# Kernel tuning notes

Hardware: AMD Instinct MI355X
Metric: run time of the kernel (lower is better)

## Reference

```python
import jax, jax.numpy as jnp
import numpy as np

B, S, H, NH = 2, 2048, 1024, 16
D = H // NH

def setup_inputs() -> dict:
    key = jax.random.key(0)
    ks = jax.random.split(key, 9)
    s = 1.0 / np.sqrt(H)
    return {
        "x": jax.random.normal(ks[0], (B, S, H), jnp.float32),
        "wq": jax.random.uniform(ks[1], (H, H), jnp.float32, -s, s),
        "bq": jax.random.uniform(ks[2], (H,), jnp.float32, -s, s),
        "wk": jax.random.uniform(ks[3], (H, H), jnp.float32, -s, s),
        "bk": jax.random.uniform(ks[4], (H,), jnp.float32, -s, s),
        "wv": jax.random.uniform(ks[5], (H, H), jnp.float32, -s, s),
        "bv": jax.random.uniform(ks[6], (H,), jnp.float32, -s, s),
        "wo": jax.random.uniform(ks[7], (H, H), jnp.float32, -s, s),
        "bo": jax.random.uniform(ks[8], (H,), jnp.float32, -s, s),
    }

def _split_heads(t):
    # [B, S, H] -> [B, NH, S, D]
    return t.reshape(B, S, NH, D).transpose(0, 2, 1, 3)

def reference(x, wq, bq, wk, bk, wv, bv, wo, bo):
    q = _split_heads(x @ wq.T + bq)
    k = _split_heads(x @ wk.T + bk)
    v = _split_heads(x @ wv.T + bv)
    scores = jnp.einsum('bhqd,bhkd->bhqk', q, k) / jnp.sqrt(jnp.float32(D))
    attn = jax.nn.softmax(scores, axis=-1)  # full [B,NH,S,S] materialized as in source
    ctx = jnp.einsum('bhqk,bhkd->bhqd', attn, v)
    concat = ctx.transpose(0, 2, 1, 3).reshape(B, S, H)
    return concat @ wo.T + bo
```

## Files before the change

kernel.cpp:

```cpp
#include <hip/hip_runtime.h>
#include <cstdint>

typedef unsigned short u16;
typedef __attribute__((ext_vector_type(8))) short short8;
typedef __attribute__((ext_vector_type(4))) float f32x4;
typedef __attribute__((ext_vector_type(4))) unsigned short ushort4v;
typedef __attribute__((ext_vector_type(4))) unsigned int uint4v;

#if __has_builtin(__builtin_amdgcn_exp2f)
#define EXP2F(x) __builtin_amdgcn_exp2f(x)
#else
#define EXP2F(x) exp2f(x)
#endif

__device__ inline u16 f2bf(float f) {
  union { float f; unsigned u; } v; v.f = f;
  unsigned u = v.u;
  return (u16)((u + 0x7fffu + ((u >> 16) & 1u)) >> 16);
}

__device__ inline float bf2f(u16 h) {
  union { unsigned u; float f; } v; v.u = ((unsigned)h) << 16;
  return v.f;
}

__device__ inline unsigned pk2bf_fast(float a, float b) {
  union { float f; unsigned u; } ua, ub; ua.f = a; ub.f = b;
  return __builtin_amdgcn_perm(ub.u + 0x8000u, ua.u + 0x8000u, 0x07060302u);
}

__device__ inline void gl2lds16(const void* g, void* l) {
  __builtin_amdgcn_global_load_lds(
      (const __attribute__((address_space(1))) unsigned int*)(unsigned long long)(uintptr_t)g,
      (__attribute__((address_space(3))) unsigned int*)(unsigned int)(uintptr_t)l,
      16, 0, 0);
}


__global__ __launch_bounds__(256) void cvt_kernel(
    const float* __restrict__ x,
    const float* __restrict__ wq, const float* __restrict__ wk,
    const float* __restrict__ wv,
    u16* __restrict__ xb, u16* __restrict__ wqb, u16* __restrict__ wkb,
    u16* __restrict__ wvb) {
  const int y = blockIdx.y;
  const int Q = 1 << 20;
  const float* src;
  u16* dst;
  if (y < 4)       { src = x + y * Q; dst = xb + y * Q; }
  else if (y == 4) { src = wq; dst = wqb; }
  else if (y == 5) { src = wk; dst = wkb; }
  else             { src = wv; dst = wvb; }
  const int i = (blockIdx.x * 256 + threadIdx.x) * 8;
  float4 a = *(const float4*)(src + i);
  float4 b = *(const float4*)(src + i + 4);
  short8 o;
  o[0] = (short)f2bf(a.x); o[1] = (short)f2bf(a.y);
  o[2] = (short)f2bf(a.z); o[3] = (short)f2bf(a.w);
  o[4] = (short)f2bf(b.x); o[5] = (short)f2bf(b.y);
  o[6] = (short)f2bf(b.z); o[7] = (short)f2bf(b.w);
  const int j = (i & ~63) | (((((i >> 3) & 7) ^ ((i >> 10) & 7))) << 3);
  *(short8*)(dst + j) = o;
}

__global__ __launch_bounds__(256, 2) void gemm_qkv(
    const u16* __restrict__ xb,
    const u16* __restrict__ wqb, const u16* __restrict__ wkb, const u16* __restrict__ wvb,
    const float* __restrict__ bq, const float* __restrict__ bk, const float* __restrict__ bv,
    u16* __restrict__ qo, u16* __restrict__ ko, u16* __restrict__ vto) {
  __shared__ u16 smem[40960];
  u16* As = smem;
  u16* Bs = smem + 16384;
  const int tid = threadIdx.x, lane = tid & 63;
  const int wid = tid >> 6;
  const int l15 = lane & 15, lg = lane >> 4;
  const int m0 = blockIdx.y * 128, n0 = blockIdx.x * 64;
  const int sw = ((l15 & 7) << 3);
  const u16* Wz[3] = {wqb, wkb, wvb};

  f32x4 acc[3][2][4] = {};

#pragma unroll
  for (int i = 0; i < 4; ++i) {
    int c = i * 256 + tid;
    gl2lds16(xb + (m0 + (c >> 3)) * 1024 + (c & 7) * 8, As + c * 8);
  }
#pragma unroll
  for (int z = 0; z < 3; ++z)
#pragma unroll
    for (int i = 0; i < 2; ++i) {
      int c = i * 256 + tid;
      gl2lds16(Wz[z] + (n0 + (c >> 3)) * 1024 + (c & 7) * 8, Bs + z * 4096 + c * 8);
    }

  for (int k0 = 0; k0 < 1024; k0 += 64) {
    const int p = (k0 >> 6) & 1;
    __syncthreads();
    if (k0 < 960) {
      u16* An = As + (1 - p) * 8192;
      u16* Bn = Bs + (1 - p) * 12288;
#pragma unroll
      for (int i = 0; i < 4; ++i) {
        int c = i * 256 + tid;
        gl2lds16(xb + (m0 + (c >> 3)) * 1024 + k0 + 64 + (c & 7) * 8, An + c * 8);
      }
#pragma unroll
      for (int z = 0; z < 3; ++z)
#pragma unroll
        for (int i = 0; i < 2; ++i) {
          int c = i * 256 + tid;
          gl2lds16(Wz[z] + (n0 + (c >> 3)) * 1024 + k0 + 64 + (c & 7) * 8, Bn + z * 4096 + c * 8);
        }
    }
    const u16* Ap = As + p * 8192;
    const u16* Bp = Bs + p * 12288;
#pragma unroll
    for (int kk = 0; kk < 2; ++kk) {
      short8 af[2], bf[3][4];
#pragma unroll
      for (int mb = 0; mb < 2; ++mb)
        af[mb] = *(const short8*)(Ap + (wid * 32 + mb * 16 + l15) * 64 + ((((kk * 4 + lg) << 3)) ^ sw));
#pragma unroll
      for (int z = 0; z < 3; ++z)
#pragma unroll
        for (int nb = 0; nb < 4; ++nb)
          bf[z][nb] = *(const short8*)(Bp + z * 4096 + (nb * 16 + l15) * 64 + ((((kk * 4 + lg) << 3)) ^ sw));
#pragma unroll
      for (int z = 0; z < 3; ++z)
#pragma unroll
        for (int mb = 0; mb < 2; ++mb)
#pragma unroll
          for (int nb = 0; nb < 4; ++nb)
            acc[z][mb][nb] = __builtin_amdgcn_mfma_f32_16x16x32_bf16(af[mb], bf[z][nb], acc[z][mb][nb], 0, 0, 0);
    }
  }

  const float cexp = 0.18033688011112042f;

#pragma unroll
  for (int mb = 0; mb < 2; ++mb)
#pragma unroll
    for (int nb = 0; nb < 4; ++nb)
#pragma unroll
      for (int r = 0; r < 4; ++r) {
        int m = m0 + wid * 32 + mb * 16 + lg * 4 + r;
        int n = n0 + nb * 16 + l15;
        float v = (acc[0][mb][nb][r] + bq[n]) * cexp;
        int b = m >> 11, s = m & 2047, hh = n >> 6, d = n & 63;
        qo[((b * 16 + hh) * 2048 + s) * 64 + d] = f2bf(v);
      }

#pragma unroll
  for (int mb = 0; mb < 2; ++mb)
#pragma unroll
    for (int nb = 0; nb < 4; ++nb)
#pragma unroll
      for (int r = 0; r < 4; ++r) {
        int m = m0 + wid * 32 + mb * 16 + lg * 4 + r;
        int n = n0 + nb * 16 + l15;
        float v = acc[1][mb][nb][r] + bk[n];
        int b = m >> 11, s = m & 2047, hh = n >> 6, d = n & 63;
        int dcol = (((d >> 3) ^ (s & 7)) << 3) | (d & 7);
        ko[((b * 16 + hh) * 2048 + s) * 64 + dcol] = f2bf(v);
      }

  __syncthreads();
  {
    u16* wbuf = smem + (wid >> 1) * 4608;
#pragma unroll
    for (int mb = 0; mb < 2; ++mb)
#pragma unroll
      for (int nb = 0; nb < 4; ++nb) {
        int n = n0 + nb * 16 + l15;
        float bn = bv[n];
        int dl = nb * 16 + l15;
#pragma unroll
        for (int r = 0; r < 4; ++r) {
          int sig = (wid & 1) * 32 + lg * 8 + mb * 4 + r;
          wbuf[dl * 72 + sig] = f2bf(acc[2][mb][nb][r] + bn);
        }
      }
    __syncthreads();
    int hh = n0 >> 6;
    int bb = m0 >> 11;
    int sbase = m0 & 2047;
#pragma unroll
    for (int i = 0; i < 4; ++i) {
      int idx = i * 256 + tid;
      int p2 = idx >> 9, rem = idx & 511;
      int dl = rem >> 3, c = rem & 7;
      short8 vv = *(const short8*)(smem + p2 * 4608 + dl * 72 + c * 8);
      int cs = c ^ (dl & 7);
      *(short8*)(vto + ((bb * 16 + hh) * 64 + dl) * 2048 + sbase + p2 * 64 + cs * 8) = vv;
    }
  }
}

__global__ __launch_bounds__(256, 2) void attn_kernel(
    const u16* __restrict__ qg, const u16* __restrict__ kg,
    const u16* __restrict__ vtg, u16* __restrict__ ctxg, u16* __restrict__ ctxlg) {
  const int h = blockIdx.x, qt = blockIdx.y, b = blockIdx.z;
  const int bh = b * 16 + h;
  const u16* Qg = qg + (bh * 2048 + qt * 128) * 64;
  const u16* Kg = kg + bh * 2048 * 64;
  const u16* Vg = vtg + bh * 64 * 2048;

  __shared__ unsigned SP32[128 * 72];
  __shared__ u16 KV[2][8192];

  const int tid = threadIdx.x, lane = tid & 63, wid = tid >> 6;
  const int l15 = lane & 15, lg = lane >> 4;
  const int row0 = wid * 32;
  const int sw = ((l15 & 7) << 3);

  short8 qf[2][2];
#pragma unroll
  for (int qtile = 0; qtile < 2; ++qtile)
#pragma unroll
    for (int kk = 0; kk < 2; ++kk)
      qf[qtile][kk] = *(const short8*)(Qg + (row0 + qtile * 16 + l15) * 64 + kk * 32 + lg * 8);

  short8 ones8;
#pragma unroll
  for (int j = 0; j < 8; ++j) ones8[j] = (short)0x3F80;

#pragma unroll
  for (int i = 0; i < 2; ++i) {
    int c = i * 256 + tid;
    gl2lds16(Kg + c * 8, &KV[0][c * 8]);
    gl2lds16(Vg + (c >> 3) * 2048 + (c & 7) * 8, &KV[0][4096 + c * 8]);
  }

  f32x4 acc[4][2] = {};
  f32x4 accl[2] = {};

  for (int kt = 0; kt < 32; ++kt) {
    const int p = kt & 1;
    __syncthreads();
    if (kt < 31) {
#pragma unroll
      for (int i = 0; i < 2; ++i) {
        int c = i * 256 + tid;
        gl2lds16(Kg + (kt + 1) * 4096 + c * 8, &KV[1 - p][c * 8]);
        gl2lds16(Vg + (c >> 3) * 2048 + (kt + 1) * 64 + (c & 7) * 8, &KV[1 - p][4096 + c * 8]);
      }
    }
    const u16* Ks = &KV[p][0];
    const u16* Vts = &KV[p][4096];

    f32x4 sc[4][2] = {};
#pragma unroll
    for (int kk = 0; kk < 2; ++kk) {
      short8 kf[4];
#pragma unroll
      for (int ktile = 0; ktile < 4; ++ktile)
        kf[ktile] = *(const short8*)(Ks + (ktile * 16 + l15) * 64 + ((((kk * 4 + lg) << 3)) ^ sw));
#pragma unroll
      for (int ktile = 0; ktile < 4; ++ktile)
#pragma unroll
        for (int qtile = 0; qtile < 2; ++qtile)
          sc[ktile][qtile] = __builtin_amdgcn_mfma_f32_16x16x32_bf16(kf[ktile], qf[qtile][kk], sc[ktile][qtile], 0, 0, 0);
    }

    short8 pf[2][2];
#pragma unroll
    for (int sl = 0; sl < 2; ++sl)
#pragma unroll
      for (int qtile = 0; qtile < 2; ++qtile) {
        union { short8 s; unsigned u[4]; } pu;
        float a0 = EXP2F(sc[sl * 2][qtile][0]),     a1 = EXP2F(sc[sl * 2][qtile][1]);
        float a2 = EXP2F(sc[sl * 2][qtile][2]),     a3 = EXP2F(sc[sl * 2][qtile][3]);
        float b0 = EXP2F(sc[sl * 2 + 1][qtile][0]), b1 = EXP2F(sc[sl * 2 + 1][qtile][1]);
        float b2 = EXP2F(sc[sl * 2 + 1][qtile][2]), b3 = EXP2F(sc[sl * 2 + 1][qtile][3]);
        pu.u[0] = pk2bf_fast(a0, a1);
        pu.u[1] = pk2bf_fast(a2, a3);
        pu.u[2] = pk2bf_fast(b0, b1);
        pu.u[3] = pk2bf_fast(b2, b3);
        pf[sl][qtile] = pu.s;
      }

#pragma unroll
    for (int sl = 0; sl < 2; ++sl) {
      short8 vf[4];
#pragma unroll
      for (int dtile = 0; dtile < 4; ++dtile)
        vf[dtile] = *(const short8*)(Vts + (dtile * 16 + l15) * 64 + ((((sl * 4 + lg) << 3)) ^ sw));
#pragma unroll
      for (int dtile = 0; dtile < 4; ++dtile)
#pragma unroll
        for (int qtile = 0; qtile < 2; ++qtile)
          acc[dtile][qtile] = __builtin_amdgcn_mfma_f32_16x16x32_bf16(vf[dtile], pf[sl][qtile], acc[dtile][qtile], 0, 0, 0);
#pragma unroll
      for (int qtile = 0; qtile < 2; ++qtile)
        accl[qtile] = __builtin_amdgcn_mfma_f32_16x16x32_bf16(ones8, pf[sl][qtile], accl[qtile], 0, 0, 0);
    }
  }

#pragma unroll
  for (int qtile = 0; qtile < 2; ++qtile) {
    float inv = 1.0f / accl[qtile][0];
#pragma unroll
    for (int dtile = 0; dtile < 4; ++dtile) {
      uint4v pk;
#pragma unroll
      for (int r = 0; r < 4; ++r) {
        float o = acc[dtile][qtile][r] * inv;
        u16 hi = f2bf(o);
        u16 lo = f2bf(o - bf2f(hi));
        pk[r] = (unsigned)hi | ((unsigned)lo << 16);
      }
      *(uint4v*)(SP32 + (row0 + qtile * 16 + l15) * 72 + dtile * 16 + lg * 4) = pk;
    }
  }
#pragma unroll
  for (int i = 0; i < 4; ++i) {
    int idx = i * 64 + lane;
    int rl = idx >> 3, c = idx & 7;
    const unsigned* src = SP32 + (row0 + rl) * 72 + c * 8;
    uint4v w0 = *(const uint4v*)(src);
    uint4v w1 = *(const uint4v*)(src + 4);
    union { unsigned u[4]; short8 s; } H, L;
    H.u[0] = __builtin_amdgcn_perm(w0[1], w0[0], 0x05040100u);
    L.u[0] = __builtin_amdgcn_perm(w0[1], w0[0], 0x07060302u);
    H.u[1] = __builtin_amdgcn_perm(w0[3], w0[2], 0x05040100u);
    L.u[1] = __builtin_amdgcn_perm(w0[3], w0[2], 0x07060302u);
    H.u[2] = __builtin_amdgcn_perm(w1[1], w1[0], 0x05040100u);
    L.u[2] = __builtin_amdgcn_perm(w1[1], w1[0], 0x07060302u);
    H.u[3] = __builtin_amdgcn_perm(w1[3], w1[2], 0x05040100u);
    L.u[3] = __builtin_amdgcn_perm(w1[3], w1[2], 0x07060302u);
    int s = qt * 128 + row0 + rl;
    int cs = c ^ (s & 7);
    long off = ((long)b * 2048 + s) * 1024 + h * 64 + cs * 8;
    *(short8*)(ctxg + off) = H.s;
    *(short8*)(ctxlg + off) = L.s;
  }
}

__global__ __launch_bounds__(256, 3) void gemm_out(
    const u16* __restrict__ ch, const u16* __restrict__ cl,
    const float* __restrict__ wo, const float* __restrict__ bo,
    float* __restrict__ out) {
  __shared__ u16 smem[24576];
  u16* Ah = smem;
  u16* Al = smem + 8192;
  u16* Bh = smem + 16384;
  u16* Bl = smem + 20480;
  const int tid = threadIdx.x, lane = tid & 63;
  const int wid = tid >> 6;
  const int l15 = lane & 15, lg = lane >> 4;
  const int m0 = blockIdx.y * 128, n0 = blockIdx.x * 64;
  const int sw = ((l15 & 7) << 3);
  const int brow = tid >> 2;
  const int bk4 = (tid & 3) * 16;

  f32x4 acc[2][4] = {};

  float4 wr0[4], wr1[4];
#pragma unroll
  for (int j = 0; j < 4; ++j)
    wr0[j] = *(const float4*)(wo + (n0 + brow) * 1024 + bk4 + j * 4);

  for (int k0 = 0; k0 < 1024; k0 += 64) {
    __syncthreads();
#pragma unroll
    for (int i = 0; i < 4; ++i) {
      int c = i * 256 + tid;
      gl2lds16(ch + (m0 + (c >> 3)) * 1024 + k0 + (c & 7) * 8, Ah + c * 8);
    }
#pragma unroll
    for (int i = 0; i < 4; ++i) {
      int c = i * 256 + tid;
      gl2lds16(cl + (m0 + (c >> 3)) * 1024 + k0 + (c & 7) * 8, Al + c * 8);
    }
    if (k0 < 960) {
#pragma unroll
      for (int j = 0; j < 4; ++j)
        wr1[j] = *(const float4*)(wo + (n0 + brow) * 1024 + k0 + 64 + bk4 + j * 4);
    }
#pragma unroll
    for (int half = 0; half < 2; ++half) {
      short8 hh, ll;
#pragma unroll
      for (int q2 = 0; q2 < 2; ++q2) {
        float4 v = wr0[half * 2 + q2];
        float vv[4] = {v.x, v.y, v.z, v.w};
#pragma unroll
        for (int e = 0; e < 4; ++e) {
          u16 hi = f2bf(vv[e]);
          u16 lo = f2bf(vv[e] - bf2f(hi));
          hh[q2 * 4 + e] = (short)hi;
          ll[q2 * 4 + e] = (short)lo;
        }
      }
      int c = (tid & 3) * 2 + half;
      int pos = brow * 64 + ((c ^ (brow & 7)) << 3);
      *(short8*)(Bh + pos) = hh;
      *(short8*)(Bl + pos) = ll;
    }
    __syncthreads();

#pragma unroll
    for (int kk = 0; kk < 2; ++kk) {
      short8 ah[2], al[2], bh[4], bl[4];
#pragma unroll
      for (int mb = 0; mb < 2; ++mb) {
        int ro = (wid * 32 + mb * 16 + l15) * 64 + ((((kk * 4 + lg) << 3)) ^ sw);
        ah[mb] = *(const short8*)(Ah + ro);
        al[mb] = *(const short8*)(Al + ro);
      }
#pragma unroll
      for (int nb = 0; nb < 4; ++nb) {
        int ro = (nb * 16 + l15) * 64 + ((((kk * 4 + lg) << 3)) ^ sw);
        bh[nb] = *(const short8*)(Bh + ro);
        bl[nb] = *(const short8*)(Bl + ro);
      }
#pragma unroll
      for (int mb = 0; mb < 2; ++mb)
#pragma unroll
        for (int nb = 0; nb < 4; ++nb) {
          acc[mb][nb] = __builtin_amdgcn_mfma_f32_16x16x32_bf16(ah[mb], bh[nb], acc[mb][nb], 0, 0, 0);
          acc[mb][nb] = __builtin_amdgcn_mfma_f32_16x16x32_bf16(al[mb], bh[nb], acc[mb][nb], 0, 0, 0);
          acc[mb][nb] = __builtin_amdgcn_mfma_f32_16x16x32_bf16(ah[mb], bl[nb], acc[mb][nb], 0, 0, 0);
        }
    }
#pragma unroll
    for (int j = 0; j < 4; ++j) wr0[j] = wr1[j];
  }

#pragma unroll
  for (int mb = 0; mb < 2; ++mb)
#pragma unroll
    for (int nb = 0; nb < 4; ++nb)
#pragma unroll
      for (int r = 0; r < 4; ++r) {
        int m = m0 + wid * 32 + mb * 16 + lg * 4 + r;
        int n = n0 + nb * 16 + l15;
        out[m * 1024 + n] = acc[mb][nb][r] + bo[n];
      }
}

extern "C" void kernel_launch(void* const* d_in, const int* in_sizes, int n_in,
                              void* d_out, int out_size, void* d_ws, size_t ws_size,
                              hipStream_t stream) {
  const float* x  = (const float*)d_in[0];
  const float* wq = (const float*)d_in[1];
  const float* bq = (const float*)d_in[2];
  const float* wk = (const float*)d_in[3];
  const float* bk = (const float*)d_in[4];
  const float* wv = (const float*)d_in[5];
  const float* bv = (const float*)d_in[6];
  const float* wo = (const float*)d_in[7];
  const float* bo = (const float*)d_in[8];

  if (ws_size < (size_t)23 * 1024 * 1024 * 2) return;
  u16* xb    = (u16*)d_ws;
  u16* wqb   = xb  + (4u << 20);
  u16* wkb   = wqb + (1u << 20);
  u16* wvb   = wkb + (1u << 20);
  u16* qb    = wvb + (1u << 20);
  u16* kb    = qb  + (4u << 20);
  u16* vtb   = kb  + (4u << 20);
  u16* ctxb  = vtb + (4u << 20);
  u16* ctxlb = xb;

  cvt_kernel<<<dim3(512, 7, 1), 256, 0, stream>>>(x, wq, wk, wv, xb, wqb, wkb, wvb);
  gemm_qkv<<<dim3(16, 32, 1), 256, 0, stream>>>(xb, wqb, wkb, wvb, bq, bk, bv, qb, kb, vtb);
  attn_kernel<<<dim3(16, 16, 2), 256, 0, stream>>>(qb, kb, vtb, ctxb, ctxlb);
  gemm_out<<<dim3(16, 32, 1), 256, 0, stream>>>(ctxb, ctxlb, wo, bo, (float*)d_out);
}
```

Before: 189.2 us.

## Switch pipeline from bf16 to fp16 and drop split-precision output projection

Converts all intermediate operands (x, weights, Q/K/V, probabilities, context) from bf16 to fp16 and uses f16 MFMA. Because fp16 has more mantissa bits, the output projection no longer needs the hi/lo split (three MFMAs per tile and a second context buffer). Wo is now pre-converted in the conversion kernel, and gemm_out becomes a single double-buffered f16 GEMM with smaller M tiles. Explicit waitcnt drains are added before barriers. The risk is fp16 overflow or range issues in unnormalized exp scores and activations.

```diff
diff --git a/kernel.cpp b/kernel.cpp
--- a/kernel.cpp
+++ b/kernel.cpp
@@ -3,9 +3,10 @@
 
 typedef unsigned short u16;
 typedef __attribute__((ext_vector_type(8))) short short8;
+typedef __attribute__((ext_vector_type(8))) _Float16 half8;
+typedef __attribute__((ext_vector_type(2))) __fp16 fp16x2;
 typedef __attribute__((ext_vector_type(4))) float f32x4;
 typedef __attribute__((ext_vector_type(4))) unsigned short ushort4v;
-typedef __attribute__((ext_vector_type(4))) unsigned int uint4v;
 
 #if __has_builtin(__builtin_amdgcn_exp2f)
 #define EXP2F(x) __builtin_amdgcn_exp2f(x)
@@ -13,20 +14,15 @@
 #define EXP2F(x) exp2f(x)
 #endif
 
-__device__ inline u16 f2bf(float f) {
-  union { float f; unsigned u; } v; v.f = f;
-  unsigned u = v.u;
-  return (u16)((u + 0x7fffu + ((u >> 16) & 1u)) >> 16);
-}
-
-__device__ inline float bf2f(u16 h) {
-  union { unsigned u; float f; } v; v.u = ((unsigned)h) << 16;
-  return v.f;
-}
-
-__device__ inline unsigned pk2bf_fast(float a, float b) {
-  union { float f; unsigned u; } ua, ub; ua.f = a; ub.f = b;
-  return __builtin_amdgcn_perm(ub.u + 0x8000u, ua.u + 0x8000u, 0x07060302u);
+#define SYNC_DRAIN() do { \
+  asm volatile("s_waitcnt vmcnt(0) lgkmcnt(0)" ::: "memory"); \
+  __syncthreads(); \
+} while (0)
+
+__device__ inline u16 f2h(float f) {
+  union { _Float16 h; u16 u; } v;
+  v.h = (_Float16)f;
+  return v.u;
 }
 
 __device__ inline void gl2lds16(const void* g, void* l) {
@@ -40,9 +36,9 @@
 __global__ __launch_bounds__(256) void cvt_kernel(
     const float* __restrict__ x,
     const float* __restrict__ wq, const float* __restrict__ wk,
-    const float* __restrict__ wv,
+    const float* __restrict__ wv, const float* __restrict__ wo,
     u16* __restrict__ xb, u16* __restrict__ wqb, u16* __restrict__ wkb,
-    u16* __restrict__ wvb) {
+    u16* __restrict__ wvb, u16* __restrict__ wob) {
   const int y = blockIdx.y;
   const int Q = 1 << 20;
   const float* src;
@@ -50,15 +46,16 @@
   if (y < 4)       { src = x + y * Q; dst = xb + y * Q; }
   else if (y == 4) { src = wq; dst = wqb; }
   else if (y == 5) { src = wk; dst = wkb; }
-  else             { src = wv; dst = wvb; }
+  else if (y == 6) { src = wv; dst = wvb; }
+  else             { src = wo; dst = wob; }
   const int i = (blockIdx.x * 256 + threadIdx.x) * 8;
   float4 a = *(const float4*)(src + i);
   float4 b = *(const float4*)(src + i + 4);
   short8 o;
-  o[0] = (short)f2bf(a.x); o[1] = (short)f2bf(a.y);
-  o[2] = (short)f2bf(a.z); o[3] = (short)f2bf(a.w);
-  o[4] = (short)f2bf(b.x); o[5] = (short)f2bf(b.y);
-  o[6] = (short)f2bf(b.z); o[7] = (short)f2bf(b.w);
+  o[0] = (short)f2h(a.x); o[1] = (short)f2h(a.y);
+  o[2] = (short)f2h(a.z); o[3] = (short)f2h(a.w);
+  o[4] = (short)f2h(b.x); o[5] = (short)f2h(b.y);
+  o[6] = (short)f2h(b.z); o[7] = (short)f2h(b.w);
   const int j = (i & ~63) | (((((i >> 3) & 7) ^ ((i >> 10) & 7))) << 3);
   *(short8*)(dst + j) = o;
 }
@@ -95,7 +92,7 @@
 
   for (int k0 = 0; k0 < 1024; k0 += 64) {
     const int p = (k0 >> 6) & 1;
-    __syncthreads();
+    SYNC_DRAIN();
     if (k0 < 960) {
       u16* An = As + (1 - p) * 8192;
       u16* Bn = Bs + (1 - p) * 12288;
@@ -116,22 +113,22 @@
     const u16* Bp = Bs + p * 12288;
 #pragma unroll
     for (int kk = 0; kk < 2; ++kk) {
-      short8 af[2], bf[3][4];
+      half8 af[2], bf[3][4];
 #pragma unroll
       for (int mb = 0; mb < 2; ++mb)
-        af[mb] = *(const short8*)(Ap + (wid * 32 + mb * 16 + l15) * 64 + ((((kk * 4 + lg) << 3)) ^ sw));
+        af[mb] = *(const half8*)(Ap + (wid * 32 + mb * 16 + l15) * 64 + ((((kk * 4 + lg) << 3)) ^ sw));
 #pragma unroll
       for (int z = 0; z < 3; ++z)
 #pragma unroll
         for (int nb = 0; nb < 4; ++nb)
-          bf[z][nb] = *(const short8*)(Bp + z * 4096 + (nb * 16 + l15) * 64 + ((((kk * 4 + lg) << 3)) ^ sw));
+          bf[z][nb] = *(const half8*)(Bp + z * 4096 + (nb * 16 + l15) * 64 + ((((kk * 4 + lg) << 3)) ^ sw));
 #pragma unroll
       for (int z = 0; z < 3; ++z)
 #pragma unroll
         for (int mb = 0; mb < 2; ++mb)
 #pragma unroll
           for (int nb = 0; nb < 4; ++nb)
-            acc[z][mb][nb] = __builtin_amdgcn_mfma_f32_16x16x32_bf16(af[mb], bf[z][nb], acc[z][mb][nb], 0, 0, 0);
+            acc[z][mb][nb] = __builtin_amdgcn_mfma_f32_16x16x32_f16(af[mb], bf[z][nb], acc[z][mb][nb], 0, 0, 0);
     }
   }
 
@@ -147,7 +144,7 @@
         int n = n0 + nb * 16 + l15;
         float v = (acc[0][mb][nb][r] + bq[n]) * cexp;
         int b = m >> 11, s = m & 2047, hh = n >> 6, d = n & 63;
-        qo[((b * 16 + hh) * 2048 + s) * 64 + d] = f2bf(v);
+        qo[((b * 16 + hh) * 2048 + s) * 64 + d] = f2h(v);
       }
 
 #pragma unroll
@@ -161,10 +158,10 @@
         float v = acc[1][mb][nb][r] + bk[n];
         int b = m >> 11, s = m & 2047, hh = n >> 6, d = n & 63;
         int dcol = (((d >> 3) ^ (s & 7)) << 3) | (d & 7);
-        ko[((b * 16 + hh) * 2048 + s) * 64 + dcol] = f2bf(v);
-      }
-
-  __syncthreads();
+        ko[((b * 16 + hh) * 2048 + s) * 64 + dcol] = f2h(v);
+      }
+
+  SYNC_DRAIN();
   {
     u16* wbuf = smem + (wid >> 1) * 4608;
 #pragma unroll
@@ -177,10 +174,10 @@
 #pragma unroll
         for (int r = 0; r < 4; ++r) {
           int sig = (wid & 1) * 32 + lg * 8 + mb * 4 + r;
-          wbuf[dl * 72 + sig] = f2bf(acc[2][mb][nb][r] + bn);
+          wbuf[dl * 72 + sig] = f2h(acc[2][mb][nb][r] + bn);
         }
       }
-    __syncthreads();
+    SYNC_DRAIN();
     int hh = n0 >> 6;
     int bb = m0 >> 11;
     int sbase = m0 & 2047;
@@ -198,14 +195,14 @@
 
 __global__ __launch_bounds__(256, 2) void attn_kernel(
     const u16* __restrict__ qg, const u16* __restrict__ kg,
-    const u16* __restrict__ vtg, u16* __restrict__ ctxg, u16* __restrict__ ctxlg) {
+    const u16* __restrict__ vtg, u16* __restrict__ ctxg) {
   const int h = blockIdx.x, qt = blockIdx.y, b = blockIdx.z;
   const int bh = b * 16 + h;
   const u16* Qg = qg + (bh * 2048 + qt * 128) * 64;
   const u16* Kg = kg + bh * 2048 * 64;
   const u16* Vg = vtg + bh * 64 * 2048;
 
-  __shared__ unsigned SP32[128 * 72];
+  __shared__ u16 SP[128 * 72];
   __shared__ u16 KV[2][8192];
 
   const int tid = threadIdx.x, lane = tid & 63, wid = tid >> 6;
@@ -213,16 +210,16 @@
   const int row0 = wid * 32;
   const int sw = ((l15 & 7) << 3);
 
-  short8 qf[2][2];
+  half8 qf[2][2];
 #pragma unroll
   for (int qtile = 0; qtile < 2; ++qtile)
 #pragma unroll
     for (int kk = 0; kk < 2; ++kk)
-      qf[qtile][kk] = *(const short8*)(Qg + (row0 + qtile * 16 + l15) * 64 + kk * 32 + lg * 8);
-
-  short8 ones8;
-#pragma unroll
-  for (int j = 0; j < 8; ++j) ones8[j] = (short)0x3F80;
+      qf[qtile][kk] = *(const half8*)(Qg + (row0 + qtile * 16 + l15) * 64 + kk * 32 + lg * 8);
+
+  half8 ones8;
+#pragma unroll
+  for (int j = 0; j < 8; ++j) ones8[j] = (_Float16)1.0f;
 
 #pragma unroll
   for (int i = 0; i < 2; ++i) {
@@ -236,7 +233,7 @@
 
   for (int kt = 0; kt < 32; ++kt) {
     const int p = kt & 1;
-    __syncthreads();
+    SYNC_DRAIN();
     if (kt < 31) {
 #pragma unroll
       for (int i = 0; i < 2; ++i) {
@@ -251,48 +248,48 @@
     f32x4 sc[4][2] = {};
 #pragma unroll
     for (int kk = 0; kk < 2; ++kk) {
-      short8 kf[4];
+      half8 kf[4];
 #pragma unroll
       for (int ktile = 0; ktile < 4; ++ktile)
-        kf[ktile] = *(const short8*)(Ks + (ktile * 16 + l15) * 64 + ((((kk * 4 + lg) << 3)) ^ sw));
+        kf[ktile] = *(const half8*)(Ks + (ktile * 16 + l15) * 64 + ((((kk * 4 + lg) << 3)) ^ sw));
 #pragma unroll
       for (int ktile = 0; ktile < 4; ++ktile)
 #pragma unroll
         for (int qtile = 0; qtile < 2; ++qtile)
-          sc[ktile][qtile] = __builtin_amdgcn_mfma_f32_16x16x32_bf16(kf[ktile], qf[qtile][kk], sc[ktile][qtile], 0, 0, 0);
-    }
-
-    short8 pf[2][2];
+          sc[ktile][qtile] = __builtin_amdgcn_mfma_f32_16x16x32_f16(kf[ktile], qf[qtile][kk], sc[ktile][qtile], 0, 0, 0);
+    }
+
+    half8 pf[2][2];
 #pragma unroll
     for (int sl = 0; sl < 2; ++sl)
 #pragma unroll
       for (int qtile = 0; qtile < 2; ++qtile) {
-        union { short8 s; unsigned u[4]; } pu;
+        union { half8 h; fp16x2 h2[4]; } pu;
         float a0 = EXP2F(sc[sl * 2][qtile][0]),     a1 = EXP2F(sc[sl * 2][qtile][1]);
         float a2 = EXP2F(sc[sl * 2][qtile][2]),     a3 = EXP2F(sc[sl * 2][qtile][3]);
         float b0 = EXP2F(sc[sl * 2 + 1][qtile][0]), b1 = EXP2F(sc[sl * 2 + 1][qtile][1]);
         float b2 = EXP2F(sc[sl * 2 + 1][qtile][2]), b3 = EXP2F(sc[sl * 2 + 1][qtile][3]);
-        pu.u[0] = pk2bf_fast(a0, a1);
-        pu.u[1] = pk2bf_fast(a2, a3);
-        pu.u[2] = pk2bf_fast(b0, b1);
-        pu.u[3] = pk2bf_fast(b2, b3);
-        pf[sl][qtile] = pu.s;
+        pu.h2[0] = __builtin_amdgcn_cvt_pkrtz(a0, a1);
+        pu.h2[1] = __builtin_amdgcn_cvt_pkrtz(a2, a3);
+        pu.h2[2] = __builtin_amdgcn_cvt_pkrtz(b0, b1);
+        pu.h2[3] = __builtin_amdgcn_cvt_pkrtz(b2, b3);
+        pf[sl][qtile] = pu.h;
       }
 
 #pragma unroll
     for (int sl = 0; sl < 2; ++sl) {
-      short8 vf[4];
+      half8 vf[4];
 #pragma unroll
       for (int dtile = 0; dtile < 4; ++dtile)
-        vf[dtile] = *(const short8*)(Vts + (dtile * 16 + l15) * 64 + ((((sl * 4 + lg) << 3)) ^ sw));
+        vf[dtile] = *(const half8*)(Vts + (dtile * 16 + l15) * 64 + ((((sl * 4 + lg) << 3)) ^ sw));
 #pragma unroll
       for (int dtile = 0; dtile < 4; ++dtile)
 #pragma unroll
         for (int qtile = 0; qtile < 2; ++qtile)
-          acc[dtile][qtile] = __builtin_amdgcn_mfma_f32_16x16x32_bf16(vf[dtile], pf[sl][qtile], acc[dtile][qtile], 0, 0, 0);
+          acc[dtile][qtile] = __builtin_amdgcn_mfma_f32_16x16x32_f16(vf[dtile], pf[sl][qtile], acc[dtile][qtile], 0, 0, 0);
 #pragma unroll
       for (int qtile = 0; qtile < 2; ++qtile)
-        accl[qtile] = __builtin_amdgcn_mfma_f32_16x16x32_bf16(ones8, pf[sl][qtile], accl[qtile], 0, 0, 0);
+        accl[qtile] = __builtin_amdgcn_mfma_f32_16x16x32_f16(ones8, pf[sl][qtile], accl[qtile], 0, 0, 0);
     }
   }
 
@@ -301,142 +298,82 @@
     float inv = 1.0f / accl[qtile][0];
 #pragma unroll
     for (int dtile = 0; dtile < 4; ++dtile) {
-      uint4v pk;
-#pragma unroll
-      for (int r = 0; r < 4; ++r) {
-        float o = acc[dtile][qtile][r] * inv;
-        u16 hi = f2bf(o);
-        u16 lo = f2bf(o - bf2f(hi));
-        pk[r] = (unsigned)hi | ((unsigned)lo << 16);
-      }
-      *(uint4v*)(SP32 + (row0 + qtile * 16 + l15) * 72 + dtile * 16 + lg * 4) = pk;
-    }
-  }
+      ushort4v pk;
+#pragma unroll
+      for (int r = 0; r < 4; ++r)
+        pk[r] = f2h(acc[dtile][qtile][r] * inv);
+      *(ushort4v*)(SP + (row0 + qtile * 16 + l15) * 72 + dtile * 16 + lg * 4) = pk;
+    }
+  }
+  SYNC_DRAIN();
 #pragma unroll
   for (int i = 0; i < 4; ++i) {
     int idx = i * 64 + lane;
     int rl = idx >> 3, c = idx & 7;
-    const unsigned* src = SP32 + (row0 + rl) * 72 + c * 8;
-    uint4v w0 = *(const uint4v*)(src);
-    uint4v w1 = *(const uint4v*)(src + 4);
-    union { unsigned u[4]; short8 s; } H, L;
-    H.u[0] = __builtin_amdgcn_perm(w0[1], w0[0], 0x05040100u);
-    L.u[0] = __builtin_amdgcn_perm(w0[1], w0[0], 0x07060302u);
-    H.u[1] = __builtin_amdgcn_perm(w0[3], w0[2], 0x05040100u);
-    L.u[1] = __builtin_amdgcn_perm(w0[3], w0[2], 0x07060302u);
-    H.u[2] = __builtin_amdgcn_perm(w1[1], w1[0], 0x05040100u);
-    L.u[2] = __builtin_amdgcn_perm(w1[1], w1[0], 0x07060302u);
-    H.u[3] = __builtin_amdgcn_perm(w1[3], w1[2], 0x05040100u);
-    L.u[3] = __builtin_amdgcn_perm(w1[3], w1[2], 0x07060302u);
+    short8 vv = *(const short8*)(SP + (row0 + rl) * 72 + c * 8);
     int s = qt * 128 + row0 + rl;
     int cs = c ^ (s & 7);
-    long off = ((long)b * 2048 + s) * 1024 + h * 64 + cs * 8;
-    *(short8*)(ctxg + off) = H.s;
-    *(short8*)(ctxlg + off) = L.s;
-  }
-}
-
-__global__ __launch_bounds__(256, 3) void gemm_out(
-    const u16* __restrict__ ch, const u16* __restrict__ cl,
-    const float* __restrict__ wo, const float* __restrict__ bo,
-    float* __restrict__ out) {
-  __shared__ u16 smem[24576];
-  u16* Ah = smem;
-  u16* Al = smem + 8192;
-  u16* Bh = smem + 16384;
-  u16* Bl = smem + 20480;
+    *(short8*)(ctxg + ((long)b * 2048 + s) * 1024 + h * 64 + cs * 8) = vv;
+  }
+}
+
+__global__ __launch_bounds__(256) void gemm_out(
+    const u16* __restrict__ cb, const u16* __restrict__ wob,
+    const float* __restrict__ bo, float* __restrict__ out) {
+  __shared__ u16 smem[16384];
+  u16* As = smem;
+  u16* Bs = smem + 8192;
   const int tid = threadIdx.x, lane = tid & 63;
   const int wid = tid >> 6;
   const int l15 = lane & 15, lg = lane >> 4;
-  const int m0 = blockIdx.y * 128, n0 = blockIdx.x * 64;
+  const int m0 = blockIdx.y * 64, n0 = blockIdx.x * 64;
   const int sw = ((l15 & 7) << 3);
-  const int brow = tid >> 2;
-  const int bk4 = (tid & 3) * 16;
-
-  f32x4 acc[2][4] = {};
-
-  float4 wr0[4], wr1[4];
-#pragma unroll
-  for (int j = 0; j < 4; ++j)
-    wr0[j] = *(const float4*)(wo + (n0 + brow) * 1024 + bk4 + j * 4);
+
+  f32x4 acc[4] = {};
+
+#pragma unroll
+  for (int i = 0; i < 2; ++i) {
+    int c = i * 256 + tid;
+    gl2lds16(cb  + (m0 + (c >> 3)) * 1024 + (c & 7) * 8, As + c * 8);
+    gl2lds16(wob + (n0 + (c >> 3)) * 1024 + (c & 7) * 8, Bs + c * 8);
+  }
 
   for (int k0 = 0; k0 < 1024; k0 += 64) {
-    __syncthreads();
-#pragma unroll
-    for (int i = 0; i < 4; ++i) {
-      int c = i * 256 + tid;
-      gl2lds16(ch + (m0 + (c >> 3)) * 1024 + k0 + (c & 7) * 8, Ah + c * 8);
-    }
-#pragma unroll
-    for (int i = 0; i < 4; ++i) {
-      int c = i * 256 + tid;
-      gl2lds16(cl + (m0 + (c >> 3)) * 1024 + k0 + (c & 7) * 8, Al + c * 8);
-    }
+    const int p = (k0 >> 6) & 1;
+    SYNC_DRAIN();
     if (k0 < 960) {
-#pragma unroll
-      for (int j = 0; j < 4; ++j)
-        wr1[j] = *(const float4*)(wo + (n0 + brow) * 1024 + k0 + 64 + bk4 + j * 4);
-    }
-#pragma unroll
-    for (int half = 0; half < 2; ++half) {
-      short8 hh, ll;
-#pragma unroll
-      for (int q2 = 0; q2 < 2; ++q2) {
-        float4 v = wr0[half * 2 + q2];
-        float vv[4] = {v.x, v.y, v.z, v.w};
-#pragma unroll
-        for (int e = 0; e < 4; ++e) {
-          u16 hi = f2bf(vv[e]);
-          u16 lo = f2bf(vv[e] - bf2f(hi));
-          hh[q2 * 4 + e] = (short)hi;
-          ll[q2 * 4 + e] = (short)lo;
-        }
-      }
-      int c = (tid & 3) * 2 + half;
-      int pos = brow * 64 + ((c ^ (brow & 7)) << 3);
-      *(short8*)(Bh + pos) = hh;
-      *(short8*)(Bl + pos) = ll;
-    }
-    __syncthreads();
-
+      u16* An = As + (1 - p) * 4096;
+      u16* Bn = Bs + (1 - p) * 4096;
+#pragma unroll
+      for (int i = 0; i < 2; ++i) {
+        int c = i * 256 + tid;
+        gl2lds16(cb  + (m0 + (c >> 3)) * 1024 + k0 + 64 + (c & 7) * 8, An + c * 8);
+        gl2lds16(wob + (n0 + (c >> 3)) * 1024 + k0 + 64 + (c & 7) * 8, Bn + c * 8);
+      }
+    }
+    const u16* Ap = As + p * 4096;
+    const u16* Bp = Bs + p * 4096;
 #pragma unroll
     for (int kk = 0; kk < 2; ++kk) {
-      short8 ah[2], al[2], bh[4], bl[4];
-#pragma unroll
-      for (int mb = 0; mb < 2; ++mb) {
-        int ro = (wid * 32 + mb * 16 + l15) * 64 + ((((kk * 4 + lg) << 3)) ^ sw);
-        ah[mb] = *(const short8*)(Ah + ro);
-        al[mb] = *(const short8*)(Al + ro);
-      }
-#pragma unroll
-      for (int nb = 0; nb < 4; ++nb) {
-        int ro = (nb * 16 + l15) * 64 + ((((kk * 4 + lg) << 3)) ^ sw);
-        bh[nb] = *(const short8*)(Bh + ro);
-        bl[nb] = *(const short8*)(Bl + ro);
-      }
-#pragma unroll
-      for (int mb = 0; mb < 2; ++mb)
-#pragma unroll
-        for (int nb = 0; nb < 4; ++nb) {
-          acc[mb][nb] = __builtin_amdgcn_mfma_f32_16x16x32_bf16(ah[mb], bh[nb], acc[mb][nb], 0, 0, 0);
-          acc[mb][nb] = __builtin_amdgcn_mfma_f32_16x16x32_bf16(al[mb], bh[nb], acc[mb][nb], 0, 0, 0);
-          acc[mb][nb] = __builtin_amdgcn_mfma_f32_16x16x32_bf16(ah[mb], bl[nb], acc[mb][nb], 0, 0, 0);
-        }
-    }
-#pragma unroll
-    for (int j = 0; j < 4; ++j) wr0[j] = wr1[j];
-  }
-
-#pragma unroll
-  for (int mb = 0; mb < 2; ++mb)
-#pragma unroll
-    for (int nb = 0; nb < 4; ++nb)
-#pragma unroll
-      for (int r = 0; r < 4; ++r) {
-        int m = m0 + wid * 32 + mb * 16 + lg * 4 + r;
-        int n = n0 + nb * 16 + l15;
-        out[m * 1024 + n] = acc[mb][nb][r] + bo[n];
-      }
+      half8 af, bf[4];
+      af = *(const half8*)(Ap + (wid * 16 + l15) * 64 + ((((kk * 4 + lg) << 3)) ^ sw));
+#pragma unroll
+      for (int nb = 0; nb < 4; ++nb)
+        bf[nb] = *(const half8*)(Bp + (nb * 16 + l15) * 64 + ((((kk * 4 + lg) << 3)) ^ sw));
+#pragma unroll
+      for (int nb = 0; nb < 4; ++nb)
+        acc[nb] = __builtin_amdgcn_mfma_f32_16x16x32_f16(af, bf[nb], acc[nb], 0, 0, 0);
+    }
+  }
+
+#pragma unroll
+  for (int nb = 0; nb < 4; ++nb)
+#pragma unroll
+    for (int r = 0; r < 4; ++r) {
+      int m = m0 + wid * 16 + lg * 4 + r;
+      int n = n0 + nb * 16 + l15;
+      out[m * 1024 + n] = acc[nb][r] + bo[n];
+    }
 }
 
 extern "C" void kernel_launch(void* const* d_in, const int* in_sizes, int n_in,
@@ -452,19 +389,19 @@
   const float* wo = (const float*)d_in[7];
   const float* bo = (const float*)d_in[8];
 
-  if (ws_size < (size_t)23 * 1024 * 1024 * 2) return;
-  u16* xb    = (u16*)d_ws;
-  u16* wqb   = xb  + (4u << 20);
-  u16* wkb   = wqb + (1u << 20);
-  u16* wvb   = wkb + (1u << 20);
-  u16* qb    = wvb + (1u << 20);
-  u16* kb    = qb  + (4u << 20);
-  u16* vtb   = kb  + (4u << 20);
-  u16* ctxb  = vtb + (4u << 20);
-  u16* ctxlb = xb;
-
-  cvt_kernel<<<dim3(512, 7, 1), 256, 0, stream>>>(x, wq, wk, wv, xb, wqb, wkb, wvb);
+  if (ws_size < (size_t)24 * 1024 * 1024 * 2) return;
+  u16* xb   = (u16*)d_ws;
+  u16* wqb  = xb  + (4u << 20);
+  u16* wkb  = wqb + (1u << 20);
+  u16* wvb  = wkb + (1u << 20);
+  u16* wob  = wvb + (1u << 20);
+  u16* qb   = wob + (1u << 20);
+  u16* kb   = qb  + (4u << 20);
+  u16* vtb  = kb  + (4u << 20);
+  u16* ctxb = vtb + (4u << 20);
+
+  cvt_kernel<<<dim3(512, 8, 1), 256, 0, stream>>>(x, wq, wk, wv, wo, xb, wqb, wkb, wvb, wob);
   gemm_qkv<<<dim3(16, 32, 1), 256, 0, stream>>>(xb, wqb, wkb, wvb, bq, bk, bv, qb, kb, vtb);
-  attn_kernel<<<dim3(16, 16, 2), 256, 0, stream>>>(qb, kb, vtb, ctxb, ctxlb);
-  gemm_out<<<dim3(16, 32, 1), 256, 0, stream>>>(ctxb, ctxlb, wo, bo, (float*)d_out);
-}
+  attn_kernel<<<dim3(16, 16, 2), 256, 0, stream>>>(qb, kb, vtb, ctxb);
+  gemm_out<<<dim3(16, 64, 1), 256, 0, stream>>>(ctxb, wob, bo, (float*)d_out);
+}
```

Result: faster. 170.8 us (median of 2 runs) (-9.7%).
